# Kernel tuning notes

Measured on AMD Instinct MI355X. Metric: run time of the kernel, lower is better.

The kernel has to match this reference:

```python
import jax, jax.numpy as jnp
import numpy as np
from jax import lax

SIGMA = 1.0          # block_elemnts.combined_sigma
BN_EPS = 1e-5


def setup_inputs() -> dict:
    key = jax.random.key(0)
    k1, k2, k3, k4 = jax.random.split(key, 4)
    B, N, T, C_in, C_out = 8, 1024, 8, 64, 64
    return {
        "points": jax.random.normal(k1, (B, N, 3), dtype=jnp.float32),
        "translations": jax.random.normal(k2, (B, T, 3), dtype=jnp.float32),
        "functions": jax.random.normal(k3, (B, N, C_in), dtype=jnp.float32),
        "k_tensor": jax.random.normal(k4, (C_out, C_in, T), dtype=jnp.float32)
            * np.sqrt(2.0 / (C_in + C_out)),  # xavier_normal_
        "gamma": jnp.ones((C_out,), dtype=jnp.float32),
        "beta": jnp.zeros((C_out,), dtype=jnp.float32),
    }


def reference(points, translations, functions, k_tensor, gamma, beta):
    denom = 2.0 * SIGMA ** 2
    # pairwise squared distances [B,N,N]
    sq = jnp.sum(points * points, axis=-1)                      # [B,N]
    dist = sq[:, :, None] + sq[:, None, :] \
        - 2.0 * jnp.einsum('bnd,bmd->bnm', points, points)      # [B,N,N]
    # interpolation matrix = Gaussian kernel of distances
    interp_rowsum = jnp.sum(jnp.exp(-dist / denom), axis=2, keepdims=True)  # [B,N,1]
    w = functions / interp_rowsum                               # [B,N,Cin]
    # b_tensor[t] = w @ k_tensor[:,:,t]^T  -> [T,B,N,Cout]
    b = jnp.einsum('bnc,oct->tbno', w, k_tensor)
    ptd = jnp.einsum('bnd,btd->tbn', points, translations)      # [T,B,N]
    tsq = jnp.sum(translations * translations, axis=2).T        # [T,B]

    B_, N_, O_ = b.shape[1], b.shape[2], b.shape[3]

    def step(acc, inputs):
        b_t, ptd_t, tsq_t = inputs                              # [B,N,O],[B,N],[B]
        dot = -2.0 * ptd_t                                      # [B,N]
        # exponent = -||p_i - p_j - t||^2 / (2*sigma^2), always <= 0
        q = jnp.exp(-(dist + dot[:, :, None] - dot[:, None, :]
                      + tsq_t[:, None, None]) / denom)          # [B,N,N]
        return acc + jnp.einsum('bnm,bmo->bno', q, b_t), None

    out, _ = lax.scan(step, jnp.zeros((B_, N_, O_), dtype=b.dtype),
                      (b, ptd, tsq))                            # [B,N,O]

    # BatchNorm1d in training mode over (B,N) per channel, then ReLU
    mean = jnp.mean(out, axis=(0, 1))
    var = jnp.var(out, axis=(0, 1))
    xn = (out - mean) * lax.rsqrt(var + BN_EPS) * gamma + beta
    return jax.nn.relu(xn)                                      # [B,N,Cout]
```

## Files before the change

### kernel.cpp

```cpp
#include <hip/hip_runtime.h>
#include <hip/hip_bf16.h>
#include <cstdint>
#include <cstddef>
#include <cstring>

#define BN_EPS 1e-5f
#define L2E 1.4426950408889634f

typedef float f32x4_t __attribute__((ext_vector_type(4)));
typedef __bf16 bf16x8_t __attribute__((ext_vector_type(8)));

__device__ __forceinline__ unsigned short f2bf(float f) {
    __hip_bfloat16 h = __float2bfloat16(f);
    return __builtin_bit_cast(unsigned short, h);
}
__device__ __forceinline__ float bf2f(unsigned short u) {
    unsigned int v = ((unsigned int)u) << 16;
    return __builtin_bit_cast(float, v);
}
__device__ __forceinline__ unsigned int pkbf(float a, float b) {
    __hip_bfloat162 h = __float22bfloat162_rn(make_float2(a, b));
    unsigned int r;
    __builtin_memcpy(&r, &h, 4);
    return r;
}

__device__ __forceinline__ void gld_lds16(void* lds, const void* gp) {
#if __has_builtin(__builtin_amdgcn_global_load_lds)
    __builtin_amdgcn_global_load_lds(
        (const __attribute__((address_space(1))) unsigned int*)gp,
        (__attribute__((address_space(3))) unsigned int*)lds, 16, 0, 0);
#else
    *(uint4*)lds = *(const uint4*)gp;
#endif
}


union SmemGP {
    struct {
        float praw[3072];
        float px[1024], py[1024], pz[1024], hq[1024];
        float part[16][128];
        float p2[16][32];
    } g;
    struct {
        unsigned short Asm[128 * 72];
        unsigned short Bsm[128 * 72];
        float sfacl[256];
    } p;
};

__global__ __launch_bounds__(256) void k_gp(const float* __restrict__ points,
                                            const float* __restrict__ trans,
                                            const float* __restrict__ funcs,
                                            const float* __restrict__ ktens,
                                            float* __restrict__ rowsum,
                                            unsigned short* __restrict__ bmatT,
                                            float* __restrict__ escale,
                                            float* __restrict__ bns) {
    __shared__ SmemGP smu;
    const int tid = threadIdx.x;

    if (blockIdx.x >= 512) {
        const int bk = blockIdx.x - 512;
        const int b  = bk & 7;
        const int mt = (bk >> 3) & 7;
        const int ct = bk >> 6;
        const int m0 = mt * 128;

        unsigned short* Asm = smu.p.Asm;
        unsigned short* Bsm = smu.p.Bsm;
        float* sfacl = smu.p.sfacl;

        if (blockIdx.x == 512 && tid < 128) bns[tid] = 0.f;

        const int wave = tid >> 6, lane = tid & 63;
        const int wr = wave >> 1, wc = wave & 1;
        const int fr = lane & 15, quad = lane >> 4;

        {
            const int tloc = tid >> 7, m = tid & 127;
            const int t = ct * 2 + tloc;
            const float tx = trans[b * 24 + t * 3], ty = trans[b * 24 + t * 3 + 1],
                        tz = trans[b * 24 + t * 3 + 2];
            const float* pp = &points[(size_t)(b * 1024 + m0 + m) * 3];
            const float ptd = pp[0] * tx + pp[1] * ty + pp[2] * tz;
            const float tsq = tx * tx + ty * ty + tz * tz;
            sfacl[tloc * 128 + m] = __expf(-ptd - 0.5f * tsq);
            escale[(size_t)(b * 8 + t) * 1024 + m0 + m] = __expf(ptd);
        }
        #pragma unroll
        for (int rep = 0; rep < 2; ++rep) {
            const int m = rep * 64 + (tid >> 2);
            const int c16 = (tid & 3) * 16;
            const float* fp = &funcs[((size_t)(b * 1024) + m0 + m) * 64 + c16];
            float4 f0 = *(const float4*)fp, f1 = *(const float4*)(fp + 4);
            float4 f2 = *(const float4*)(fp + 8), f3 = *(const float4*)(fp + 12);
            uint4 p0, p1;
            p0.x = pkbf(f0.x, f0.y); p0.y = pkbf(f0.z, f0.w);
            p0.z = pkbf(f1.x, f1.y); p0.w = pkbf(f1.z, f1.w);
            p1.x = pkbf(f2.x, f2.y); p1.y = pkbf(f2.z, f2.w);
            p1.z = pkbf(f3.x, f3.y); p1.w = pkbf(f3.z, f3.w);
            *(uint4*)&Asm[m * 72 + c16] = p0;
            *(uint4*)&Asm[m * 72 + c16 + 8] = p1;
        }
        #pragma unroll
        for (int rep = 0; rep < 4; ++rep) {
            const int col = rep * 32 + (tid >> 3);
            const int c8  = (tid & 7) * 8;
            const int g   = ct * 128 + col;
            const int t   = g >> 6, o = g & 63;
            const float* kt = &ktens[(size_t)(o * 64 + c8) * 8 + t];
            uint4 v;
            v.x = pkbf(kt[0], kt[8]);
            v.y = pkbf(kt[16], kt[24]);
            v.z = pkbf(kt[32], kt[40]);
            v.w = pkbf(kt[48], kt[56]);
            *(uint4*)&Bsm[col * 72 + c8] = v;
        }
        __syncthreads();

        f32x4_t acc[4][4];
        #pragma unroll
        for (int i = 0; i < 4; ++i)
            #pragma unroll
            for (int j = 0; j < 4; ++j) acc[i][j] = f32x4_t{0.f, 0.f, 0.f, 0.f};

        #pragma unroll
        for (int s = 0; s < 2; ++s) {
            uint4 afr[4], bfr[4];
            #pragma unroll
            for (int i = 0; i < 4; ++i)
                afr[i] = *(const uint4*)&Asm[(wr * 64 + i * 16 + fr) * 72 + s * 32 + quad * 8];
            #pragma unroll
            for (int j = 0; j < 4; ++j)
                bfr[j] = *(const uint4*)&Bsm[(wc * 64 + j * 16 + fr) * 72 + s * 32 + quad * 8];
            #pragma unroll
            for (int i = 0; i < 4; ++i)
                #pragma unroll
                for (int j = 0; j < 4; ++j)
                    acc[i][j] = __builtin_amdgcn_mfma_f32_16x16x32_bf16(
                        __builtin_bit_cast(bf16x8_t, afr[i]),
                        __builtin_bit_cast(bf16x8_t, bfr[j]),
                        acc[i][j], 0, 0, 0);
        }

        #pragma unroll
        for (int i = 0; i < 4; ++i) {
            #pragma unroll
            for (int j = 0; j < 4; ++j) {
                const int colg = ct * 128 + wc * 64 + j * 16 + fr;
                const int mb = wr * 64 + i * 16 + quad * 4;
                uint2 pk;
                pk.x = pkbf(acc[i][j][0] * sfacl[wc * 128 + mb + 0],
                            acc[i][j][1] * sfacl[wc * 128 + mb + 1]);
                pk.y = pkbf(acc[i][j][2] * sfacl[wc * 128 + mb + 2],
                            acc[i][j][3] * sfacl[wc * 128 + mb + 3]);
                *(uint2*)&bmatT[(size_t)(b * 512 + colg) * 1024 + m0 + mb] = pk;
            }
        }
        return;
    }

    float* praw = smu.g.praw;
    float* px = smu.g.px; float* py = smu.g.py;
    float* pz = smu.g.pz; float* hq = smu.g.hq;
    float (*part)[128] = smu.g.part;
    float (*p2)[32] = smu.g.p2;

    const int b  = blockIdx.x & 7;
    const int n0 = (blockIdx.x >> 3) * 16;

    for (int i = tid; i < 3072; i += 256) praw[i] = points[b * 3072 + i];
    __syncthreads();
    for (int n = tid; n < 1024; n += 256) {
        float x = praw[n * 3], y = praw[n * 3 + 1], z = praw[n * 3 + 2];
        px[n] = x; py[n] = y; pz[n] = z;
        hq[n] = -0.5f * L2E * (x * x + y * y + z * z);
    }
    __syncthreads();

    const int rhalf = tid >> 7;
    const int c0 = (tid & 127) * 8;
    float vx[8], vy[8], vz[8], vh[8];
    *(float4*)&vx[0] = *(const float4*)&px[c0];
    *(float4*)&vx[4] = *(const float4*)&px[c0 + 4];
    *(float4*)&vy[0] = *(const float4*)&py[c0];
    *(float4*)&vy[4] = *(const float4*)&py[c0 + 4];
    *(float4*)&vz[0] = *(const float4*)&pz[c0];
    *(float4*)&vz[4] = *(const float4*)&pz[c0 + 4];
    *(float4*)&vh[0] = *(const float4*)&hq[c0];
    *(float4*)&vh[4] = *(const float4*)&hq[c0 + 4];

    #pragma unroll
    for (int u = 0; u < 8; ++u) {
        const int rl = u * 2 + rhalf;
        const int row = n0 + rl;
        const float rx = L2E * px[row], ry = L2E * py[row], rz = L2E * pz[row];
        const float hr = hq[row];
        float ssum = 0.f;
        #pragma unroll
        for (int j = 0; j < 8; ++j)
            ssum += __builtin_amdgcn_exp2f(hr + vh[j] + rx * vx[j]
                                           + ry * vy[j] + rz * vz[j]);
        part[rl][tid & 127] = ssum;
    }
    __syncthreads();
    #pragma unroll
    for (int rep = 0; rep < 2; ++rep) {
        const int row = rep * 8 + (tid >> 5), c4l = (tid & 31) * 4;
        float4 p = *(const float4*)&part[row][c4l];
        p2[row][tid & 31] = p.x + p.y + p.z + p.w;
    }
    __syncthreads();
    if (tid < 16) {
        float s = 0.f;
        #pragma unroll
        for (int q = 0; q < 8; ++q) {
            float4 v = *(const float4*)&p2[tid][q * 4];
            s += v.x + v.y + v.z + v.w;
        }
        rowsum[b * 1024 + n0 + tid] = s;
    }
}

__global__ __launch_bounds__(256, 2) void k_gemm(const float* __restrict__ points,
                                                 const unsigned short* __restrict__ bmatT,
                                                 const float* __restrict__ escale,
                                                 const float* __restrict__ rowsum,
                                                 unsigned short* __restrict__ He2) {
    __shared__ unsigned short Bs[3][8192];
    __shared__ float escT[1024];
    __shared__ float4 mp[256];

    const int b  = blockIdx.x & 7;
    const int rt = (blockIdx.x >> 3) & 7;
    const int z  = blockIdx.x >> 6;
    const int ogp = z & 1;
    const int kh  = z >> 1;
    const int n0 = rt * 128;
    const int kb = kh * 256;

    const int tid  = threadIdx.x;
    const int wave = tid >> 6, lane = tid & 63;

    const unsigned short* gB = bmatT + (size_t)(b * 512 + ogp * 32) * 1024 + kb;

    const int r16 = lane >> 2;
    const int kq  = lane & 3;
    const int gsw = kq ^ (r16 & 3);

    const int fr = lane & 15;
    const int quad = lane >> 4;
    const int swoff = (quad ^ (fr & 3)) << 4;
    const int row_base = wave * 32;

    float rx0, ry0, rz0, rh0, rx1, ry1, rz1, rh1;
    {
        const float* p0 = &points[(size_t)(b * 1024 + n0 + row_base + fr) * 3];
        const float x0 = p0[0], y0 = p0[1], z0 = p0[2];
        rh0 = -0.5f * L2E * (x0 * x0 + y0 * y0 + z0 * z0);
        rx0 = L2E * x0; ry0 = L2E * y0; rz0 = L2E * z0;
        const float* p1 = &points[(size_t)(b * 1024 + n0 + row_base + 16 + fr) * 3];
        const float x1 = p1[0], y1 = p1[1], z1 = p1[2];
        rh1 = -0.5f * L2E * (x1 * x1 + y1 * y1 + z1 * z1);
        rx1 = L2E * x1; ry1 = L2E * y1; rz1 = L2E * z1;
    }
    {
        const int t = tid >> 5, r4 = (tid & 31) * 4;
        float4 ev = *(const float4*)&escale[(size_t)(b * 8 + t) * 1024 + n0 + r4];
        const float* pp = &points[(size_t)(b * 1024 + kb + tid) * 3];
        const float x = pp[0], y = pp[1], zz = pp[2];
        const float rs = rowsum[b * 1024 + kb + tid];
        *(float4*)&escT[t * 128 + r4] = ev;
        mp[tid] = make_float4(x, y, zz,
                              -0.5f * L2E * (x * x + y * y + zz * zz)
                              - __builtin_amdgcn_logf(rs));
    }
    __builtin_amdgcn_sched_barrier(0);
    #pragma unroll
    for (int i = 0; i < 4; ++i) {
        const int seg = wave * 4 + i;
        const int tt = seg >> 1, oh = (seg & 1) * 16;
        gld_lds16((char*)Bs[0] + seg * 1024 + lane * 16,
                  gB + (size_t)(tt * 64 + oh + r16) * 1024 + gsw * 8);
    }
    asm volatile("s_waitcnt lgkmcnt(0)" ::: "memory");
    __builtin_amdgcn_s_barrier();

    f32x4_t acc[2][16];
    #pragma unroll
    for (int i = 0; i < 2; ++i)
        #pragma unroll
        for (int j = 0; j < 16; ++j) acc[i][j] = f32x4_t{0.f, 0.f, 0.f, 0.f};

    #pragma unroll
    for (int kk = 0; kk < 8; ++kk) {
        const int cur = kk % 3;
        if (kk < 7) {
            const int nxt = (kk + 1) % 3;
            const int k0n = (kk + 1) * 32;
            #pragma unroll
            for (int i = 0; i < 4; ++i) {
                const int seg = wave * 4 + i;
                const int tt = seg >> 1, oh = (seg & 1) * 16;
                gld_lds16((char*)Bs[nxt] + seg * 1024 + lane * 16,
                          gB + (size_t)(tt * 64 + oh + r16) * 1024 + k0n + gsw * 8);
            }
        }
        uint4 afr0, afr1;
        {
            const int mbase = kk * 32 + quad * 8;
            float e0[8], e1[8];
            #pragma unroll
            for (int j = 0; j < 8; ++j) {
                const float4 m4 = mp[mbase + j];
                e0[j] = __builtin_amdgcn_exp2f(rh0 + m4.w + rx0 * m4.x
                                               + ry0 * m4.y + rz0 * m4.z);
                e1[j] = __builtin_amdgcn_exp2f(rh1 + m4.w + rx1 * m4.x
                                               + ry1 * m4.y + rz1 * m4.z);
            }
            afr0.x = pkbf(e0[0], e0[1]); afr0.y = pkbf(e0[2], e0[3]);
            afr0.z = pkbf(e0[4], e0[5]); afr0.w = pkbf(e0[6], e0[7]);
            afr1.x = pkbf(e1[0], e1[1]); afr1.y = pkbf(e1[2], e1[3]);
            afr1.z = pkbf(e1[4], e1[5]); afr1.w = pkbf(e1[6], e1[7]);
        }
        if (kk < 7) asm volatile("s_waitcnt vmcnt(4)" ::: "memory");
        else        asm volatile("s_waitcnt vmcnt(0)" ::: "memory");
        __builtin_amdgcn_s_barrier();
        #pragma unroll
        for (int j = 0; j < 16; ++j) {
            uint4 bfr = *(const uint4*)((const char*)Bs[cur] + (j * 16 + fr) * 64 + swoff);
            acc[0][j] = __builtin_amdgcn_mfma_f32_16x16x32_bf16(
                __builtin_bit_cast(bf16x8_t, afr0),
                __builtin_bit_cast(bf16x8_t, bfr), acc[0][j], 0, 0, 0);
            acc[1][j] = __builtin_amdgcn_mfma_f32_16x16x32_bf16(
                __builtin_bit_cast(bf16x8_t, afr1),
                __builtin_bit_cast(bf16x8_t, bfr), acc[1][j], 0, 0, 0);
        }
    }

    const int oo = lane & 15;
    unsigned short* dst = He2 + (size_t)kh * 524288
                              + (size_t)(b * 1024 + n0) * 64 + ogp * 32;
    #pragma unroll
    for (int i = 0; i < 2; ++i) {
        const int rb = row_base + i * 16 + quad * 4;
        float s0[4] = {0.f, 0.f, 0.f, 0.f}, s1[4] = {0.f, 0.f, 0.f, 0.f};
        #pragma unroll
        for (int t = 0; t < 8; ++t) {
            const float4 ev = *(const float4*)&escT[t * 128 + rb];
            s0[0] += ev.x * acc[i][2 * t][0]; s1[0] += ev.x * acc[i][2 * t + 1][0];
            s0[1] += ev.y * acc[i][2 * t][1]; s1[1] += ev.y * acc[i][2 * t + 1][1];
            s0[2] += ev.z * acc[i][2 * t][2]; s1[2] += ev.z * acc[i][2 * t + 1][2];
            s0[3] += ev.w * acc[i][2 * t][3]; s1[3] += ev.w * acc[i][2 * t + 1][3];
        }
        #pragma unroll
        for (int r = 0; r < 4; ++r) {
            dst[(size_t)(rb + r) * 64 + oo] = f2bf(s0[r]);
            dst[(size_t)(rb + r) * 64 + 16 + oo] = f2bf(s1[r]);
        }
    }
}

__global__ __launch_bounds__(256) void k_fin(const unsigned short* __restrict__ He2,
                                             float* __restrict__ out,
                                             float* __restrict__ bns) {
    __shared__ float s1[16][64], s2[16][64];
    const int tid = threadIdx.x;
    const int vb = ((blockIdx.x & 7) << 5) | (blockIdx.x >> 3);
    float a0 = 0.f, a1 = 0.f, a2 = 0.f, a3 = 0.f;
    float q0 = 0.f, q1 = 0.f, q2 = 0.f, q3 = 0.f;
    #pragma unroll
    for (int it = 0; it < 2; ++it) {
        const size_t idx = (size_t)vb * 512 + it * 256 + tid;
        float4 s = make_float4(0.f, 0.f, 0.f, 0.f);
        #pragma unroll
        for (int p = 0; p < 4; ++p) {
            ushort4 u = *(const ushort4*)(He2 + (size_t)p * 524288 + idx * 4);
            s.x += bf2f(u.x); s.y += bf2f(u.y); s.z += bf2f(u.z); s.w += bf2f(u.w);
        }
        ((float4*)out)[idx] = s;
        a0 += s.x; a1 += s.y; a2 += s.z; a3 += s.w;
        q0 += s.x * s.x; q1 += s.y * s.y; q2 += s.z * s.z; q3 += s.w * s.w;
    }
    const int g = tid >> 4, o4 = (tid & 15) * 4;
    *(float4*)&s1[g][o4] = make_float4(a0, a1, a2, a3);
    *(float4*)&s2[g][o4] = make_float4(q0, q1, q2, q3);
    __syncthreads();
    if (tid < 64) {
        float sa = 0.f, sb = 0.f;
        #pragma unroll
        for (int r = 0; r < 16; ++r) { sa += s1[r][tid]; sb += s2[r][tid]; }
        atomicAdd(&bns[tid], sa);
        atomicAdd(&bns[64 + tid], sb);
    }
}

__global__ __launch_bounds__(256) void k_bn(float* __restrict__ out,
                                            const float* __restrict__ bns,
                                            const float* __restrict__ gamma,
                                            const float* __restrict__ beta) {
    const int vb = ((blockIdx.x & 7) << 6) | (blockIdx.x >> 3);
    const int i = vb * 256 + threadIdx.x;
    const int o4 = (i & 15) * 4;
    float4 x = ((float4*)out)[i];
    const float4 s  = *(const float4*)&bns[o4];
    const float4 s2 = *(const float4*)&bns[64 + o4];
    const float4 gm = *(const float4*)&gamma[o4];
    const float4 bt = *(const float4*)&beta[o4];
    const float invn = 1.f / 8192.f;
    float m, v, w;
    m = s.x * invn; v = s2.x * invn - m * m; w = __frsqrt_rn(v + BN_EPS) * gm.x;
    x.x = fmaxf((x.x - m) * w + bt.x, 0.f);
    m = s.y * invn; v = s2.y * invn - m * m; w = __frsqrt_rn(v + BN_EPS) * gm.y;
    x.y = fmaxf((x.y - m) * w + bt.y, 0.f);
    m = s.z * invn; v = s2.z * invn - m * m; w = __frsqrt_rn(v + BN_EPS) * gm.z;
    x.z = fmaxf((x.z - m) * w + bt.z, 0.f);
    m = s.w * invn; v = s2.w * invn - m * m; w = __frsqrt_rn(v + BN_EPS) * gm.w;
    x.w = fmaxf((x.w - m) * w + bt.w, 0.f);
    ((float4*)out)[i] = x;
}

extern "C" void kernel_launch(void* const* d_in, const int* in_sizes, int n_in,
                              void* d_out, int out_size, void* d_ws, size_t ws_size,
                              hipStream_t stream) {
    const float* points = (const float*)d_in[0];
    const float* trans  = (const float*)d_in[1];
    const float* funcs  = (const float*)d_in[2];
    const float* ktens  = (const float*)d_in[3];
    const float* gamma  = (const float*)d_in[4];
    const float* beta   = (const float*)d_in[5];
    float* out = (float*)d_out;

    float* ws      = (float*)d_ws;
    float* escale  = ws;
    float* bns     = escale + 65536;
    float* rowsum  = bns + 128;
    unsigned short* He2   = (unsigned short*)(rowsum + 8192);
    unsigned short* bmatT = He2 + 2097152;

    k_gp<<<768, 256, 0, stream>>>(points, trans, funcs, ktens,
                                  rowsum, bmatT, escale, bns);
    k_gemm<<<512, 256, 0, stream>>>(points, bmatT, escale, rowsum, He2);
    k_fin<<<256, 256, 0, stream>>>(He2, out, bns);
    k_bn<<<512, 256, 0, stream>>>(out, bns, gamma, beta);
}
```

Baseline: 102.6 us.

## Retile Gaussian GEMM to 256 rows by 16 output channels per block

```diff
diff --git a/kernel.cpp b/kernel.cpp
--- a/kernel.cpp
+++ b/kernel.cpp
@@ -229,22 +229,21 @@
                                                  const float* __restrict__ escale,
                                                  const float* __restrict__ rowsum,
                                                  unsigned short* __restrict__ He2) {
-    __shared__ unsigned short Bs[3][8192];
-    __shared__ float escT[1024];
+    __shared__ unsigned short Bs[3][4096];
+    __shared__ float escT[2048];
     __shared__ float4 mp[256];
 
     const int b  = blockIdx.x & 7;
-    const int rt = (blockIdx.x >> 3) & 7;
-    const int z  = blockIdx.x >> 6;
-    const int ogp = z & 1;
-    const int kh  = z >> 1;
-    const int n0 = rt * 128;
+    const int rt = (blockIdx.x >> 3) & 3;
+    const int og = (blockIdx.x >> 5) & 3;
+    const int kh = blockIdx.x >> 7;
+    const int n0 = rt * 256;
     const int kb = kh * 256;
 
     const int tid  = threadIdx.x;
     const int wave = tid >> 6, lane = tid & 63;
 
-    const unsigned short* gB = bmatT + (size_t)(b * 512 + ogp * 32) * 1024 + kb;
+    const unsigned short* gB = bmatT + (size_t)(b * 512 + og * 16) * 1024 + kb;
 
     const int r16 = lane >> 2;
     const int kq  = lane & 3;
@@ -253,46 +252,45 @@
     const int fr = lane & 15;
     const int quad = lane >> 4;
     const int swoff = (quad ^ (fr & 3)) << 4;
-    const int row_base = wave * 32;
-
-    float rx0, ry0, rz0, rh0, rx1, ry1, rz1, rh1;
+    const int row_base = wave * 64;
+
+    float rx[4], ry[4], rz[4], rh[4];
+    #pragma unroll
+    for (int i = 0; i < 4; ++i) {
+        const float* p = &points[(size_t)(b * 1024 + n0 + row_base + i * 16 + fr) * 3];
+        const float x = p[0], y = p[1], z = p[2];
+        rh[i] = -0.5f * L2E * (x * x + y * y + z * z);
+        rx[i] = L2E * x; ry[i] = L2E * y; rz[i] = L2E * z;
+    }
+    #pragma unroll
+    for (int rep = 0; rep < 2; ++rep) {
+        const int t = tid >> 5, r4 = rep * 128 + (tid & 31) * 4;
+        *(float4*)&escT[t * 256 + r4] =
+            *(const float4*)&escale[(size_t)(b * 8 + t) * 1024 + n0 + r4];
+    }
     {
-        const float* p0 = &points[(size_t)(b * 1024 + n0 + row_base + fr) * 3];
-        const float x0 = p0[0], y0 = p0[1], z0 = p0[2];
-        rh0 = -0.5f * L2E * (x0 * x0 + y0 * y0 + z0 * z0);
-        rx0 = L2E * x0; ry0 = L2E * y0; rz0 = L2E * z0;
-        const float* p1 = &points[(size_t)(b * 1024 + n0 + row_base + 16 + fr) * 3];
-        const float x1 = p1[0], y1 = p1[1], z1 = p1[2];
-        rh1 = -0.5f * L2E * (x1 * x1 + y1 * y1 + z1 * z1);
-        rx1 = L2E * x1; ry1 = L2E * y1; rz1 = L2E * z1;
-    }
-    {
-        const int t = tid >> 5, r4 = (tid & 31) * 4;
-        float4 ev = *(const float4*)&escale[(size_t)(b * 8 + t) * 1024 + n0 + r4];
         const float* pp = &points[(size_t)(b * 1024 + kb + tid) * 3];
         const float x = pp[0], y = pp[1], zz = pp[2];
         const float rs = rowsum[b * 1024 + kb + tid];
-        *(float4*)&escT[t * 128 + r4] = ev;
         mp[tid] = make_float4(x, y, zz,
                               -0.5f * L2E * (x * x + y * y + zz * zz)
                               - __builtin_amdgcn_logf(rs));
     }
     __builtin_amdgcn_sched_barrier(0);
     #pragma unroll
-    for (int i = 0; i < 4; ++i) {
-        const int seg = wave * 4 + i;
-        const int tt = seg >> 1, oh = (seg & 1) * 16;
+    for (int i = 0; i < 2; ++i) {
+        const int seg = wave * 2 + i;
         gld_lds16((char*)Bs[0] + seg * 1024 + lane * 16,
-                  gB + (size_t)(tt * 64 + oh + r16) * 1024 + gsw * 8);
+                  gB + (size_t)(seg * 64 + r16) * 1024 + gsw * 8);
     }
     asm volatile("s_waitcnt lgkmcnt(0)" ::: "memory");
     __builtin_amdgcn_s_barrier();
 
-    f32x4_t acc[2][16];
-    #pragma unroll
-    for (int i = 0; i < 2; ++i)
-        #pragma unroll
-        for (int j = 0; j < 16; ++j) acc[i][j] = f32x4_t{0.f, 0.f, 0.f, 0.f};
+    f32x4_t acc[4][8];
+    #pragma unroll
+    for (int i = 0; i < 4; ++i)
+        #pragma unroll
+        for (int j = 0; j < 8; ++j) acc[i][j] = f32x4_t{0.f, 0.f, 0.f, 0.f};
 
     #pragma unroll
     for (int kk = 0; kk < 8; ++kk) {
@@ -301,65 +299,63 @@
             const int nxt = (kk + 1) % 3;
             const int k0n = (kk + 1) * 32;
             #pragma unroll
-            for (int i = 0; i < 4; ++i) {
-                const int seg = wave * 4 + i;
-                const int tt = seg >> 1, oh = (seg & 1) * 16;
+            for (int i = 0; i < 2; ++i) {
+                const int seg = wave * 2 + i;
                 gld_lds16((char*)Bs[nxt] + seg * 1024 + lane * 16,
-                          gB + (size_t)(tt * 64 + oh + r16) * 1024 + k0n + gsw * 8);
+                          gB + (size_t)(seg * 64 + r16) * 1024 + k0n + gsw * 8);
             }
         }
-        uint4 afr0, afr1;
+        uint4 afr[4];
         {
             const int mbase = kk * 32 + quad * 8;
-            float e0[8], e1[8];
+            float e[4][8];
             #pragma unroll
             for (int j = 0; j < 8; ++j) {
                 const float4 m4 = mp[mbase + j];
-                e0[j] = __builtin_amdgcn_exp2f(rh0 + m4.w + rx0 * m4.x
-                                               + ry0 * m4.y + rz0 * m4.z);
-                e1[j] = __builtin_amdgcn_exp2f(rh1 + m4.w + rx1 * m4.x
-                                               + ry1 * m4.y + rz1 * m4.z);
+                #pragma unroll
+                for (int i = 0; i < 4; ++i)
+                    e[i][j] = __builtin_amdgcn_exp2f(rh[i] + m4.w + rx[i] * m4.x
+                                                     + ry[i] * m4.y + rz[i] * m4.z);
             }
-            afr0.x = pkbf(e0[0], e0[1]); afr0.y = pkbf(e0[2], e0[3]);
-            afr0.z = pkbf(e0[4], e0[5]); afr0.w = pkbf(e0[6], e0[7]);
-            afr1.x = pkbf(e1[0], e1[1]); afr1.y = pkbf(e1[2], e1[3]);
-            afr1.z = pkbf(e1[4], e1[5]); afr1.w = pkbf(e1[6], e1[7]);
-        }
-        if (kk < 7) asm volatile("s_waitcnt vmcnt(4)" ::: "memory");
+            #pragma unroll
+            for (int i = 0; i < 4; ++i) {
+                afr[i].x = pkbf(e[i][0], e[i][1]);
+                afr[i].y = pkbf(e[i][2], e[i][3]);
+                afr[i].z = pkbf(e[i][4], e[i][5]);
+                afr[i].w = pkbf(e[i][6], e[i][7]);
+            }
+        }
+        if (kk < 7) asm volatile("s_waitcnt vmcnt(2)" ::: "memory");
         else        asm volatile("s_waitcnt vmcnt(0)" ::: "memory");
         __builtin_amdgcn_s_barrier();
         #pragma unroll
-        for (int j = 0; j < 16; ++j) {
+        for (int j = 0; j < 8; ++j) {
             uint4 bfr = *(const uint4*)((const char*)Bs[cur] + (j * 16 + fr) * 64 + swoff);
-            acc[0][j] = __builtin_amdgcn_mfma_f32_16x16x32_bf16(
-                __builtin_bit_cast(bf16x8_t, afr0),
-                __builtin_bit_cast(bf16x8_t, bfr), acc[0][j], 0, 0, 0);
-            acc[1][j] = __builtin_amdgcn_mfma_f32_16x16x32_bf16(
-                __builtin_bit_cast(bf16x8_t, afr1),
-                __builtin_bit_cast(bf16x8_t, bfr), acc[1][j], 0, 0, 0);
-        }
-    }
-
-    const int oo = lane & 15;
+            #pragma unroll
+            for (int i = 0; i < 4; ++i)
+                acc[i][j] = __builtin_amdgcn_mfma_f32_16x16x32_bf16(
+                    __builtin_bit_cast(bf16x8_t, afr[i]),
+                    __builtin_bit_cast(bf16x8_t, bfr), acc[i][j], 0, 0, 0);
+        }
+    }
+
     unsigned short* dst = He2 + (size_t)kh * 524288
-                              + (size_t)(b * 1024 + n0) * 64 + ogp * 32;
-    #pragma unroll
-    for (int i = 0; i < 2; ++i) {
+                              + (size_t)(b * 1024 + n0) * 64 + og * 16 + fr;
+    #pragma unroll
+    for (int i = 0; i < 4; ++i) {
         const int rb = row_base + i * 16 + quad * 4;
-        float s0[4] = {0.f, 0.f, 0.f, 0.f}, s1[4] = {0.f, 0.f, 0.f, 0.f};
+        float s[4] = {0.f, 0.f, 0.f, 0.f};
         #pragma unroll
         for (int t = 0; t < 8; ++t) {
-            const float4 ev = *(const float4*)&escT[t * 128 + rb];
-            s0[0] += ev.x * acc[i][2 * t][0]; s1[0] += ev.x * acc[i][2 * t + 1][0];
-            s0[1] += ev.y * acc[i][2 * t][1]; s1[1] += ev.y * acc[i][2 * t + 1][1];
-            s0[2] += ev.z * acc[i][2 * t][2]; s1[2] += ev.z * acc[i][2 * t + 1][2];
-            s0[3] += ev.w * acc[i][2 * t][3]; s1[3] += ev.w * acc[i][2 * t + 1][3];
-        }
-        #pragma unroll
-        for (int r = 0; r < 4; ++r) {
-            dst[(size_t)(rb + r) * 64 + oo] = f2bf(s0[r]);
-            dst[(size_t)(rb + r) * 64 + 16 + oo] = f2bf(s1[r]);
-        }
+            const float4 ev = *(const float4*)&escT[t * 256 + rb];
+            s[0] += ev.x * acc[i][t][0];
+            s[1] += ev.y * acc[i][t][1];
+            s[2] += ev.z * acc[i][t][2];
+            s[3] += ev.w * acc[i][t][3];
+        }
+        #pragma unroll
+        for (int r = 0; r < 4; ++r)
+            dst[(size_t)(rb + r) * 64] = f2bf(s[r]);
     }
 }
 
```

Measured after the change: 105.2 us. 1.03x slower.
